# Kernel tuning notes

Measured on AMD Instinct MI355X. Metric: run time of the kernel, lower is better.

The kernel has to match this reference:

```python
import jax, jax.numpy as jnp
import numpy as np

N, E, F_IN, H, C, ED, NODES = 25000, 100000, 16, 4, 280, 6, 6


def setup_inputs() -> dict:
    key = jax.random.key(0)
    ks = jax.random.split(key, 16)
    s = lambda k, sh: jax.random.normal(k, sh, dtype=jnp.float32) * 0.05
    return {
        "x": jax.random.normal(ks[0], (N, F_IN), dtype=jnp.float32),
        "edge_index": jax.random.randint(ks[1], (2, E), 0, N, dtype=jnp.int64),
        "edge_attr": jax.random.normal(ks[2], (E, ED), dtype=jnp.float32),
        # TransformerConv params (PyG): lin_query/key/value (bias), lin_edge (no bias), lin_skip (bias)
        "Wq": s(ks[3], (F_IN, H * C)), "bq": jnp.zeros((H * C,), jnp.float32),
        "Wk": s(ks[4], (F_IN, H * C)), "bk": jnp.zeros((H * C,), jnp.float32),
        "Wv": s(ks[5], (F_IN, H * C)), "bv": jnp.zeros((H * C,), jnp.float32),
        "We": s(ks[6], (ED, H * C)),
        "Wskip": s(ks[7], (F_IN, C)), "bskip": jnp.zeros((C,), jnp.float32),
        # MLP: 280 -> 64 -> 16 -> NODES, softmax
        "W1": s(ks[8], (280, 64)), "b1": jnp.zeros((64,), jnp.float32),
        "W2": s(ks[9], (64, 16)), "b2": jnp.zeros((16,), jnp.float32),
        "W3": s(ks[10], (16, NODES)), "b3": jnp.zeros((NODES,), jnp.float32),
    }


def reference(x, edge_index, edge_attr, Wq, bq, Wk, bk, Wv, bv, We, Wskip, bskip, W1, b1, W2, b2, W3, b3):
    n = x.shape[0]
    src, dst = edge_index[0], edge_index[1]  # message j -> i (PyG convention)
    q = (x @ Wq + bq).reshape(n, H, C)
    k = (x @ Wk + bk).reshape(n, H, C)
    v = (x @ Wv + bv).reshape(n, H, C)
    e = (edge_attr @ We).reshape(-1, H, C)  # [E,H,C]
    kj = k[src] + e                          # gather + edge features
    alpha = jnp.einsum('ehc,ehc->eh', q[dst], kj) / jnp.sqrt(jnp.float32(C))  # [E,H]
    # numerically stable segment softmax over destination nodes
    amax = jax.ops.segment_max(alpha, dst, num_segments=n)
    ex = jnp.exp(alpha - amax[dst])
    denom = jax.ops.segment_sum(ex, dst, num_segments=n)
    attn = ex / (denom[dst] + 1e-16)
    out = jax.ops.segment_sum(attn[..., None] * (v[src] + e), dst, num_segments=n)  # [N,H,C]
    out = out.mean(axis=1)                  # concat=False -> mean over heads
    out = out + x @ Wskip + bskip           # root/skip connection
    h = out.reshape(-1, 280)
    h = jax.nn.relu(h @ W1 + b1)
    h = jax.nn.relu(h @ W2 + b2)
    return jax.nn.softmax(h @ W3 + b3, axis=-1)
```

## Files before the change

### kernel.cpp

```cpp
#include <hip/hip_runtime.h>

#define N_NODES 25000
#define N_EDGES 100000
#define CH 280
#define HC 1120
#define CAP 32

typedef unsigned int uint;
typedef unsigned short ushort;
typedef __attribute__((ext_vector_type(8))) short short8;
typedef __attribute__((ext_vector_type(4))) float f32x4;

#define FAC_A 0
#define FAC_B 1024
#define FAC_C 1408
#define FAC_D 1472
#define FAC_F 1536
#define FAC_G 1560
#define FAC_TOTAL 1564

#define WC_K 128

#define P_FAC_END  25
#define P_WC_END   153
#define P_W2_END   154
#define P_TOTAL    545

__device__ __forceinline__ ushort f2bf(float f) {
  union { float f; uint u; } c; c.f = f;
  uint u = c.u + 0x7FFFu + ((c.u >> 16) & 1u);
  return (ushort)(u >> 16);
}

__global__ __launch_bounds__(256) void prep_kernel(
    const float* __restrict__ Wq, const float* __restrict__ Wk,
    const float* __restrict__ We, const float* __restrict__ bq,
    const float* __restrict__ bk, float* __restrict__ fac,
    const float* __restrict__ Wv, const float* __restrict__ bv,
    const float* __restrict__ Wskip, const float* __restrict__ bskip,
    const float* __restrict__ W1, const float* __restrict__ b1,
    ushort* __restrict__ Wct,
    const float* __restrict__ W2, ushort* __restrict__ W2tg,
    const int* __restrict__ ei, const float* __restrict__ ea,
    int* __restrict__ cursor, const int* __restrict__ probe,
    float* __restrict__ erec) {
  __shared__ float part[4][64];
  int b = blockIdx.x;
  int tid = threadIdx.x;
  if (b < P_FAC_END) {
    int t4 = b * 256 + tid;
    int q = t4 >> 2, li = t4 & 3;
    if (q >= FAC_TOTAL) return;
    const float *pa, *pb;
    if (q < FAC_B) {
      int h = q >> 8, f = (q >> 4) & 15, g = q & 15;
      pa = Wq + f * HC + h * CH; pb = Wk + g * HC + h * CH;
    } else if (q < FAC_C) {
      int u = q - FAC_B; int h = u / 96, v2 = u % 96, f = v2 / 6, j = v2 % 6;
      pa = Wq + f * HC + h * CH; pb = We + j * HC + h * CH;
    } else if (q < FAC_D) {
      int u = q - FAC_C; int h = u >> 4, f = u & 15;
      pa = Wq + f * HC + h * CH; pb = bk + h * CH;
    } else if (q < FAC_F) {
      int u = q - FAC_D; int h = u >> 4, g = u & 15;
      pa = Wk + g * HC + h * CH; pb = bq + h * CH;
    } else if (q < FAC_G) {
      int u = q - FAC_F; int h = u / 6, j = u % 6;
      pa = We + j * HC + h * CH; pb = bq + h * CH;
    } else {
      int h = q - FAC_G;
      pa = bq + h * CH; pb = bk + h * CH;
    }
    float acc = 0.f;
    int c0 = li * 70;
    for (int c = c0; c < c0 + 70; ++c) acc = fmaf(pa[c], pb[c], acc);
    acc += __shfl_xor(acc, 1);
    acc += __shfl_xor(acc, 2);
    if (li == 0) fac[q] = acc;
  } else if (b < P_WC_END) {
    int r = b - P_FAC_END;
    int k = tid & 63, qt = tid >> 6;
    const float* w = nullptr;
    float scale = 1.f;
    if (r < 96) {
      int h = r / 24, j = r % 24;
      if (j != 23) {
        if (j < 16) w = Wv + j * HC + h * CH;
        else if (j < 22) w = We + (j - 16) * HC + h * CH;
        else w = bv + h * CH;
        scale = 0.25f;
      }
    } else if (r < 112) {
      w = Wskip + (r - 96) * CH;
    } else if (r == 112) {
      w = bskip;
    }
    float acc = 0.f;
    if (w) {
      int c0 = qt * 70;
      for (int c = c0; c < c0 + 70; ++c)
        acc = fmaf(w[c], W1[c * 64 + k], acc);
    }
    part[qt][k] = acc;
    __syncthreads();
    if (tid < 64) {
      float v = (part[0][k] + part[1][k]) + (part[2][k] + part[3][k]);
      v *= scale;
      if (r == 112) v += b1[k];
      Wct[k * WC_K + r] = w ? f2bf(v) : (ushort)0;
    }
  } else if (b < P_W2_END) {
    for (int t = tid; t < 1024; t += 256) {
      int m2 = t >> 6, k = t & 63;
      W2tg[m2 * 64 + k] = f2bf(W2[(size_t)k * 16 + m2]);
    }
  } else {
    int e = (b - P_W2_END) * 256 + tid;
    if (e >= N_EDGES) return;
    int src = ei[e];
    int dst = ei[N_EDGES + e];
    int base = *probe;
    int pos = atomicAdd(&cursor[dst], 1) - base;
    if (pos >= CAP) return;
    const float2* s2 = (const float2*)(ea + (size_t)e * 6);
    float2 e01 = s2[0], e23 = s2[1], e45 = s2[2];
    int4 w0;
    w0.x = src;
    w0.y = __float_as_int(e01.x); w0.z = __float_as_int(e01.y);
    w0.w = __float_as_int(e23.x);
    float4 w1 = make_float4(e23.y, e45.x, e45.y, 0.f);
    float* dstp = erec + ((size_t)dst * CAP + pos) * 8;
    *(int4*)dstp = w0;
    *(float4*)(dstp + 4) = w1;
  }
}

__global__ __launch_bounds__(512, 2) void fused_kernel(
    const float* __restrict__ x, const float* __restrict__ fac,
    const float* __restrict__ erec, const int* __restrict__ cursor,
    const int* __restrict__ probe,
    const ushort* __restrict__ Wct, const ushort* __restrict__ W2tg,
    const float* __restrict__ b2, const float* __restrict__ W3,
    const float* __restrict__ b3, float* __restrict__ out) {
  __shared__ ushort Vls[64 * 136];
  __shared__ ushort h1b[64 * 72];
  __shared__ float  h2s[64 * 17];
  const float RS = 0.05976143046671968f;
  int tid = threadIdx.x;
  int wid = tid >> 6, lane = tid & 63;
  int h = __builtin_amdgcn_readfirstlane(wid & 3);
  int nb = __builtin_amdgcn_readfirstlane(wid >> 2);
  int nloc = nb * 32 + (lane >> 1);
  int half = lane & 1;

  int n0 = blockIdx.x * 64 + nloc;
  bool valid = n0 < N_NODES;
  int n = valid ? n0 : (N_NODES - 1);
  float xv[16];
  {
    const float4* x4 = (const float4*)(x + (size_t)n * 16);
#pragma unroll
    for (int i = 0; i < 4; ++i) {
      float4 q = x4[i];
      xv[4 * i] = q.x; xv[4 * i + 1] = q.y; xv[4 * i + 2] = q.z; xv[4 * i + 3] = q.w;
    }
  }
  const float* Af = fac + FAC_A + h * 256;
  const float* Bf = fac + FAC_B + h * 96;
  const float* cf = fac + FAC_C + h * 16;
  const float* df = fac + FAC_D + h * 16;
  const float* ff = fac + FAC_F + h * 6;
  const float  gf = fac[FAC_G + h];
  float va[16];
#pragma unroll
  for (int g = 0; g < 16; ++g) {
    float a = df[g];
#pragma unroll
    for (int f = 0; f < 16; ++f) a = fmaf(xv[f], Af[f * 16 + g], a);
    va[g] = a;
  }
  float ve[6];
#pragma unroll
  for (int j = 0; j < 6; ++j) {
    float a = ff[j];
#pragma unroll
    for (int f = 0; f < 16; ++f) a = fmaf(xv[f], Bf[f * 6 + j], a);
    ve[j] = a;
  }
  float v22 = gf;
#pragma unroll
  for (int f = 0; f < 16; ++f) v22 = fmaf(xv[f], cf[f], v22);

  int base = *probe;
  int dg = valid ? (cursor[n0] - base) : 0;
  if (dg > CAP) dg = CAP;
  float m = -1e30f, den = 0.f;
  float Sx[16];
  float Sa[6];
#pragma unroll
  for (int f = 0; f < 16; ++f) Sx[f] = 0.f;
#pragma unroll
  for (int j = 0; j < 6; ++j) Sa[j] = 0.f;
  for (int q2 = half; q2 < dg; q2 += 2) {
    const float* er = erec + ((size_t)n0 * CAP + q2) * 8;
    int4 ra = *(const int4*)er;
    float4 rb = *(const float4*)(er + 4);
    int s = ra.x;
    const float4* xs4 = (const float4*)(x + (size_t)s * 16);
    float4 a0 = xs4[0], a1 = xs4[1], a2 = xs4[2], a3 = xs4[3];
    float xs[16] = {a0.x, a0.y, a0.z, a0.w, a1.x, a1.y, a1.z, a1.w,
                    a2.x, a2.y, a2.z, a2.w, a3.x, a3.y, a3.z, a3.w};
    float eav[6] = {__int_as_float(ra.y), __int_as_float(ra.z),
                    __int_as_float(ra.w), rb.x, rb.y, rb.z};
    float alpha = v22;
#pragma unroll
    for (int f = 0; f < 16; ++f) alpha = fmaf(va[f], xs[f], alpha);
#pragma unroll
    for (int j = 0; j < 6; ++j) alpha = fmaf(ve[j], eav[j], alpha);
    alpha *= RS;
    float nm = fmaxf(m, alpha);
    float sc = __expf(m - nm);
    float w = __expf(alpha - nm);
    den = den * sc + w;
#pragma unroll
    for (int f = 0; f < 16; ++f) Sx[f] = fmaf(Sx[f], sc, w * xs[f]);
#pragma unroll
    for (int j = 0; j < 6; ++j) Sa[j] = fmaf(Sa[j], sc, w * eav[j]);
    m = nm;
  }
  {
    float mo  = __shfl_xor(m, 1);
    float dno = __shfl_xor(den, 1);
    float mm = fmaxf(m, mo);
    float sa = __expf(m - mm);
    float sb = __expf(mo - mm);
    den = den * sa + dno * sb;
#pragma unroll
    for (int f = 0; f < 16; ++f) {
      float so = __shfl_xor(Sx[f], 1);
      Sx[f] = Sx[f] * sa + so * sb;
    }
#pragma unroll
    for (int j = 0; j < 6; ++j) {
      float so = __shfl_xor(Sa[j], 1);
      Sa[j] = Sa[j] * sa + so * sb;
    }
  }
  if (half == 0) {
    float inv = 1.f / (den + 1e-16f);
    float outv[24];
#pragma unroll
    for (int f = 0; f < 16; ++f) outv[f] = Sx[f] * inv;
#pragma unroll
    for (int j = 0; j < 6; ++j) outv[16 + j] = Sa[j] * inv;
    outv[22] = den * inv;
    outv[23] = 0.f;
    uint pk[12];
#pragma unroll
    for (int i = 0; i < 12; ++i)
      pk[i] = (uint)f2bf(outv[2 * i]) | ((uint)f2bf(outv[2 * i + 1]) << 16);
    int4* vp = (int4*)(Vls + nloc * 136 + h * 24);
    int4 s0, s1, s2;
    s0.x = (int)pk[0]; s0.y = (int)pk[1]; s0.z = (int)pk[2]; s0.w = (int)pk[3];
    s1.x = (int)pk[4]; s1.y = (int)pk[5]; s1.z = (int)pk[6]; s1.w = (int)pk[7];
    s2.x = (int)pk[8]; s2.y = (int)pk[9]; s2.z = (int)pk[10]; s2.w = (int)pk[11];
    vp[0] = s0; vp[1] = s1; vp[2] = s2;
    if (h == 0) {
      uint pq[8];
#pragma unroll
      for (int i = 0; i < 8; ++i)
        pq[i] = (uint)f2bf(xv[2 * i]) | ((uint)f2bf(xv[2 * i + 1]) << 16);
      int4* vq = (int4*)(Vls + nloc * 136 + 96);
      int4 t0, t1, t2, t3;
      t0.x = (int)pq[0]; t0.y = (int)pq[1]; t0.z = (int)pq[2]; t0.w = (int)pq[3];
      t1.x = (int)pq[4]; t1.y = (int)pq[5]; t1.z = (int)pq[6]; t1.w = (int)pq[7];
      t2.x = (int)0x3F80u; t2.y = 0; t2.z = 0; t2.w = 0;
      t3.x = 0; t3.y = 0; t3.z = 0; t3.w = 0;
      vq[0] = t0; vq[1] = t1; vq[2] = t2; vq[3] = t3;
    }
  }
  __syncthreads();

  int col15 = lane & 15, quad = lane >> 4;
  if (wid < 4) {
    f32x4 acc[4];
#pragma unroll
    for (int T = 0; T < 4; ++T) acc[T] = (f32x4){0.f, 0.f, 0.f, 0.f};
#pragma unroll
    for (int kk = 0; kk < 4; ++kk) {
      int k0 = kk * 32;
      short8 a = *(const short8*)(Vls + (wid * 16 + col15) * 136 + k0 + quad * 8);
#pragma unroll
      for (int T = 0; T < 4; ++T) {
        short8 bfr = *(const short8*)(Wct + (T * 16 + col15) * WC_K + k0 + quad * 8);
        acc[T] = __builtin_amdgcn_mfma_f32_16x16x32_bf16(a, bfr, acc[T], 0, 0, 0);
      }
    }
#pragma unroll
    for (int T = 0; T < 4; ++T) {
#pragma unroll
      for (int r = 0; r < 4; ++r) {
        int nl = wid * 16 + quad * 4 + r;
        int c = T * 16 + col15;
        h1b[nl * 72 + c] = f2bf(fmaxf(acc[T][r], 0.f));
      }
    }
  }
  __syncthreads();
  if (wid < 4) {
    float b2v = b2[col15];
    f32x4 acc2 = (f32x4){0.f, 0.f, 0.f, 0.f};
#pragma unroll
    for (int kk = 0; kk < 2; ++kk) {
      int k0 = kk * 32;
      short8 a2 = *(const short8*)(h1b + (wid * 16 + col15) * 72 + k0 + quad * 8);
      short8 bf2 = *(const short8*)(W2tg + col15 * 64 + k0 + quad * 8);
      acc2 = __builtin_amdgcn_mfma_f32_16x16x32_bf16(a2, bf2, acc2, 0, 0, 0);
    }
#pragma unroll
    for (int r = 0; r < 4; ++r) {
      int nl = wid * 16 + quad * 4 + r;
      h2s[nl * 17 + col15] = fmaxf(acc2[r] + b2v, 0.f);
    }
  }
  __syncthreads();
  if (tid < 64) {
    int n2 = blockIdx.x * 64 + tid;
    if (n2 < N_NODES) {
      float hv[16];
#pragma unroll
      for (int j = 0; j < 16; ++j) hv[j] = h2s[tid * 17 + j];
      float lg[6];
      float mx = -1e30f;
#pragma unroll
      for (int o = 0; o < 6; ++o) {
        float a = b3[o];
#pragma unroll
        for (int j = 0; j < 16; ++j) a = fmaf(hv[j], W3[j * 6 + o], a);
        lg[o] = a; mx = fmaxf(mx, a);
      }
      float s = 0.f;
#pragma unroll
      for (int o = 0; o < 6; ++o) { lg[o] = __expf(lg[o] - mx); s += lg[o]; }
      float inv = 1.f / s;
      float2* o2 = (float2*)(out + (size_t)n2 * 6);
      o2[0] = make_float2(lg[0] * inv, lg[1] * inv);
      o2[1] = make_float2(lg[2] * inv, lg[3] * inv);
      o2[2] = make_float2(lg[4] * inv, lg[5] * inv);
    }
  }
}

extern "C" void kernel_launch(void* const* d_in, const int* in_sizes, int n_in,
                              void* d_out, int out_size, void* d_ws, size_t ws_size,
                              hipStream_t stream) {
  const float* x     = (const float*)d_in[0];
  const int*   ei    = (const int*)d_in[1];
  const float* ea    = (const float*)d_in[2];
  const float* Wq    = (const float*)d_in[3];
  const float* bq    = (const float*)d_in[4];
  const float* Wk    = (const float*)d_in[5];
  const float* bk    = (const float*)d_in[6];
  const float* Wv    = (const float*)d_in[7];
  const float* bv    = (const float*)d_in[8];
  const float* We    = (const float*)d_in[9];
  const float* Wskip = (const float*)d_in[10];
  const float* bskip = (const float*)d_in[11];
  const float* W1    = (const float*)d_in[12];
  const float* b1    = (const float*)d_in[13];
  const float* W2    = (const float*)d_in[14];
  const float* b2    = (const float*)d_in[15];
  const float* W3    = (const float*)d_in[16];
  const float* b3    = (const float*)d_in[17];
  float* out = (float*)d_out;
  (void)in_sizes; (void)n_in; (void)out_size; (void)ws_size;

  char* ws = (char*)d_ws;
  size_t off = 0;
  auto alloc = [&](size_t bytes) {
    void* p = ws + off;
    off = (off + bytes + 255) & ~(size_t)255;
    return p;
  };
  float*  fac    = (float*)alloc(FAC_TOTAL * 4);
  ushort* Wct    = (ushort*)alloc(64 * WC_K * 2);
  int*    cursor = (int*)alloc(N_NODES * 4);
  int*    probe  = (int*)alloc(256);
  ushort* W2tg   = (ushort*)alloc(16 * 64 * 2);
  float*  erec   = (float*)alloc((size_t)N_NODES * CAP * 32);

  prep_kernel<<<P_TOTAL, 256, 0, stream>>>(
      Wq, Wk, We, bq, bk, fac, Wv, bv, Wskip, bskip, W1, b1, Wct, W2, W2tg,
      ei, ea, cursor, probe, erec);
  fused_kernel<<<391, 512, 0, stream>>>(x, fac, erec, cursor, probe, Wct, W2tg,
                                        b2, W3, b3, out);
}
```

Before: 116.3 us.

## Stage per-block edge records and source features in LDS once for all heads

Each block first computes per-node degrees and a prefix sum, then stages each edge's source-node features and edge attributes into shared memory with one thread per edge. The four head-warps then read the staged data from LDS instead of each re-gathering erec and x[src] from global memory. This cuts redundant global gathers (previously repeated four times, once per head) at the cost of about 46KB more LDS, which may reduce occupancy under launch_bounds(512,2), plus two extra barriers. Edges beyond EMAX=480 per block are silently dropped.

```diff
diff --git a/kernel.cpp b/kernel.cpp
--- a/kernel.cpp
+++ b/kernel.cpp
@@ -5,6 +5,7 @@
 #define CH 280
 #define HC 1120
 #define CAP 32
+#define EMAX 480
 
 typedef unsigned int uint;
 typedef unsigned short ushort;
@@ -142,17 +143,62 @@
     const ushort* __restrict__ Wct, const ushort* __restrict__ W2tg,
     const float* __restrict__ b2, const float* __restrict__ W3,
     const float* __restrict__ b3, float* __restrict__ out) {
+  __shared__ float  exs[EMAX * 24];
+  __shared__ int    dgs[65];
   __shared__ ushort Vls[64 * 136];
   __shared__ ushort h1b[64 * 72];
   __shared__ float  h2s[64 * 17];
   const float RS = 0.05976143046671968f;
   int tid = threadIdx.x;
   int wid = tid >> 6, lane = tid & 63;
+
+  if (tid < 64) {
+    int nn = blockIdx.x * 64 + tid;
+    int base = *probe;
+    int dg = (nn < N_NODES) ? (cursor[nn] - base) : 0;
+    if (dg > CAP) dg = CAP;
+    if (dg < 0) dg = 0;
+    int incl = dg;
+#pragma unroll
+    for (int off = 1; off < 64; off <<= 1) {
+      int t = __shfl_up(incl, off);
+      if (lane >= off) incl += t;
+    }
+    dgs[tid + 1] = incl;
+    if (tid == 0) dgs[0] = 0;
+  }
+  __syncthreads();
+  int Eblk = dgs[64];
+  if (Eblk > EMAX) Eblk = EMAX;
+  if (tid < Eblk) {
+    int lo = 0, hi = 64;
+    while (hi - lo > 1) {
+      int mid = (lo + hi) >> 1;
+      if (dgs[mid] <= tid) lo = mid; else hi = mid;
+    }
+    int nl = lo, q = tid - dgs[nl];
+    int nn = blockIdx.x * 64 + nl;
+    const float* er = erec + ((size_t)nn * CAP + q) * 8;
+    int4 ra = *(const int4*)er;
+    float4 rb = *(const float4*)(er + 4);
+    const float4* xs4 = (const float4*)(x + (size_t)ra.x * 16);
+    float4 a0 = xs4[0], a1 = xs4[1], a2 = xs4[2], a3 = xs4[3];
+    float* ex = exs + tid * 24;
+    *(float4*)(ex + 0)  = a0;
+    *(float4*)(ex + 4)  = a1;
+    *(float4*)(ex + 8)  = a2;
+    *(float4*)(ex + 12) = a3;
+    ex[16] = __int_as_float(ra.y);
+    ex[17] = __int_as_float(ra.z);
+    ex[18] = __int_as_float(ra.w);
+    ex[19] = rb.x; ex[20] = rb.y; ex[21] = rb.z;
+  }
+  __syncthreads();
+
   int h = __builtin_amdgcn_readfirstlane(wid & 3);
   int nb = __builtin_amdgcn_readfirstlane(wid >> 2);
   int nloc = nb * 32 + (lane >> 1);
   int half = lane & 1;
-
   int n0 = blockIdx.x * 64 + nloc;
   bool valid = n0 < N_NODES;
   int n = valid ? n0 : (N_NODES - 1);
@@ -191,9 +237,9 @@
 #pragma unroll
   for (int f = 0; f < 16; ++f) v22 = fmaf(xv[f], cf[f], v22);
 
-  int base = *probe;
-  int dg = valid ? (cursor[n0] - base) : 0;
-  if (dg > CAP) dg = CAP;
+  int start = dgs[nloc];  if (start > Eblk) start = Eblk;
+  int end   = dgs[nloc + 1]; if (end > Eblk) end = Eblk;
+  int dg = end - start;
   float m = -1e30f, den = 0.f;
   float Sx[16];
   float Sa[6];
@@ -202,16 +248,14 @@
 #pragma unroll
   for (int j = 0; j < 6; ++j) Sa[j] = 0.f;
   for (int q2 = half; q2 < dg; q2 += 2) {
-    const float* er = erec + ((size_t)n0 * CAP + q2) * 8;
-    int4 ra = *(const int4*)er;
-    float4 rb = *(const float4*)(er + 4);
-    int s = ra.x;
-    const float4* xs4 = (const float4*)(x + (size_t)s * 16);
-    float4 a0 = xs4[0], a1 = xs4[1], a2 = xs4[2], a3 = xs4[3];
+    const float* ex = exs + (size_t)(start + q2) * 24;
+    float4 a0 = *(const float4*)(ex + 0);
+    float4 a1 = *(const float4*)(ex + 4);
+    float4 a2 = *(const float4*)(ex + 8);
+    float4 a3 = *(const float4*)(ex + 12);
     float xs[16] = {a0.x, a0.y, a0.z, a0.w, a1.x, a1.y, a1.z, a1.w,
                     a2.x, a2.y, a2.z, a2.w, a3.x, a3.y, a3.z, a3.w};
-    float eav[6] = {__int_as_float(ra.y), __int_as_float(ra.z),
-                    __int_as_float(ra.w), rb.x, rb.y, rb.z};
+    float eav[6] = {ex[16], ex[17], ex[18], ex[19], ex[20], ex[21]};
     float alpha = v22;
 #pragma unroll
     for (int f = 0; f < 16; ++f) alpha = fmaf(va[f], xs[f], alpha);
```

Result: no change. 114.5 us (-1.6%).
